# Performance work log

Hardware: AMD Instinct MI355X
Metric: run time of the kernel (lower is better)

## Reference

```python
import jax, jax.numpy as jnp
import numpy as np

# config (matches init_kwargs)
B, CIN, P, G = 8, 3, 16, 16          # batch, channels, patch, grid (img 256)
N = G * G                            # 256 tokens
D, NH, HD = 768, 12, 64              # hidden, heads, head_dim
L, E, K, HE = 4, 8, 2, 2048          # depth, experts, top_k, expert hidden
BN, FREQ = 128, 256                  # patch-embed bottleneck, timestep freq dim
EPS = 1e-6


def rms(x, w):
    return x * jax.lax.rsqrt(jnp.mean(x * x, axis=-1, keepdims=True) + EPS) * w


def rope_tables():
    # 2D RoPE: row/col grid coords, row-major token order
    half = HD // 2
    inv = 1.0 / (10000.0 ** (jnp.arange(0, half, 2, dtype=jnp.float32) / half))
    pos = jnp.arange(N)
    ph = (pos // G).astype(jnp.float32)
    pw = (pos % G).astype(jnp.float32)
    ah = jnp.repeat(ph[:, None] * inv, 2, axis=-1)   # (N, half)
    aw = jnp.repeat(pw[:, None] * inv, 2, axis=-1)
    ang = jnp.concatenate([ah, aw], axis=-1)          # (N, HD)
    return jnp.cos(ang)[None, None], jnp.sin(ang)[None, None]  # (1,1,N,HD)


def apply_rope(x, cos, sin):
    xp = x.reshape(*x.shape[:-1], HD // 2, 2)
    xr = jnp.stack([-xp[..., 1], xp[..., 0]], axis=-1).reshape(x.shape)
    return x * cos + xr * sin


def _forward(x, t, task_id, modality_id, pe1_w, pe1_b, pe2_w, pe2_b,
             t1_w, t1_b, t2_w, t2_b, task_tab, mod_tab,
             qkv_w, proj_w, qn_w, kn_w, norm1_w, norm2_w, adaln_w, adaln_b,
             router_w, moe_w1, moe_w2, moe_w3,
             fnorm_w, fada_w, fada_b, fproj_w, fproj_b):
    # PatchEmbed (bottleneck): conv(k=p,s=p) == linear over flattened (C,p,p) patches
    xp = x.reshape(B, CIN, G, P, G, P).transpose(0, 2, 4, 1, 3, 5).reshape(B, N, CIN * P * P)
    h = jax.nn.gelu(xp @ pe1_w + pe1_b, approximate=False) @ pe2_w + pe2_b  # (B,N,D)

    # TimestepEmbedder
    half = FREQ // 2
    freqs = jnp.exp(-jnp.log(10000.0) * jnp.arange(half, dtype=jnp.float32) / half)
    te = t[:, None] * freqs
    te = jnp.concatenate([jnp.cos(te), jnp.sin(te)], axis=-1)                # (B,FREQ)
    temb = jax.nn.silu(te @ t1_w + t1_b) @ t2_w + t2_b
    c = temb + task_tab[task_id] + mod_tab[modality_id]                      # (B,D)

    cos, sin = rope_tables()
    scale = 1.0 / np.sqrt(HD)

    def block(xb, p):
        qkvw, projw, qnw, knw, n1w, n2w, aw, ab, rw, w1, w2, w3 = p
        mod = (jax.nn.silu(c) @ aw + ab)[:, None, :]                         # (B,1,6D)
        sm, scm, gm, sp, scp, gp = jnp.split(mod, 6, axis=-1)
        # attention branch
        hh = rms(xb, n1w) * (1 + scm) + sm
        qkv = (hh @ qkvw).reshape(B, N, 3, NH, HD).transpose(2, 0, 3, 1, 4)
        q, k, v = qkv[0], qkv[1], qkv[2]                                     # (B,NH,N,HD)
        q = apply_rope(rms(q, qnw), cos, sin)
        k = apply_rope(rms(k, knw), cos, sin)
        att = jax.nn.softmax(jnp.einsum('bhnd,bhmd->bhnm', q, k) * scale, axis=-1)
        o = jnp.einsum('bhnm,bhmd->bhnd', att, v).transpose(0, 2, 1, 3).reshape(B, N, D)
        xb = xb + gm * (o @ projw)
        # MoE SwiGLU FFN branch: dense all-expert compute + gated combine
        hh = rms(xb, n2w) * (1 + scp) + sp
        hf = hh.reshape(B * N, D)
        logits = hf @ rw                                                     # (T,E)
        tv, ti = jax.lax.top_k(logits, K)
        gw = jax.nn.softmax(tv, axis=-1)                                     # (T,K)
        gates = jnp.sum(jax.nn.one_hot(ti, E, dtype=hf.dtype) * gw[..., None], axis=1)  # (T,E)
        h1 = jnp.einsum('td,edh->teh', hf, w1)
        h3 = jnp.einsum('td,edh->teh', hf, w3)
        y = jnp.einsum('teh,ehd->ted', jax.nn.silu(h1) * h3, w2)
        moe = jnp.einsum('ted,te->td', y, gates).reshape(B, N, D)
        xb = xb + gp * moe
        return xb, None

    params = (qkv_w, proj_w, qn_w, kn_w, norm1_w, norm2_w,
              adaln_w, adaln_b, router_w, moe_w1, moe_w2, moe_w3)
    h, _ = jax.lax.scan(block, h, params)

    fmod = (jax.nn.silu(c) @ fada_w + fada_b)[:, None, :]
    fs, fsc = jnp.split(fmod, 2, axis=-1)
    h = rms(h, fnorm_w) * (1 + fsc) + fs
    return h @ fproj_w + fproj_b                                             # (B,N,P*P*CIN)


def setup_inputs() -> dict:
    key = jax.random.key(0)
    ks = iter(jax.random.split(key, 40))
    r = lambda shape: jax.random.normal(next(ks), shape, jnp.float32) * 0.02
    return {
        'x': jax.random.normal(next(ks), (B, CIN, G * P, G * P), jnp.float32),
        't': jax.random.uniform(next(ks), (B,), jnp.float32) * 1000.0,
        'task_id': jax.random.randint(next(ks), (B,), 0, 2),
        'modality_id': jax.random.randint(next(ks), (B,), 0, 2),
        'pe1_w': r((CIN * P * P, BN)), 'pe1_b': jnp.zeros((BN,)),
        'pe2_w': r((BN, D)), 'pe2_b': jnp.zeros((D,)),
        't1_w': r((FREQ, D)), 't1_b': jnp.zeros((D,)),
        't2_w': r((D, D)), 't2_b': jnp.zeros((D,)),
        'task_tab': r((2, D)), 'mod_tab': r((2, D)),
        'qkv_w': r((L, D, 3 * D)), 'proj_w': r((L, D, D)),
        'qn_w': jnp.ones((L, HD)), 'kn_w': jnp.ones((L, HD)),
        'norm1_w': jnp.ones((L, D)), 'norm2_w': jnp.ones((L, D)),
        'adaln_w': r((L, D, 6 * D)), 'adaln_b': jnp.zeros((L, 6 * D)),
        'router_w': r((L, D, E)),
        'moe_w1': r((L, E, D, HE)), 'moe_w2': r((L, E, HE, D)), 'moe_w3': r((L, E, D, HE)),
        'fnorm_w': jnp.ones((D,)), 'fada_w': r((D, 2 * D)), 'fada_b': jnp.zeros((2 * D,)),
        'fproj_w': r((D, P * P * CIN)), 'fproj_b': jnp.zeros((P * P * CIN,)),
    }


def reference(x, t, task_id, modality_id, pe1_w, pe1_b, pe2_w, pe2_b,
              t1_w, t1_b, t2_w, t2_b, task_tab, mod_tab,
              qkv_w, proj_w, qn_w, kn_w, norm1_w, norm2_w, adaln_w, adaln_b,
              router_w, moe_w1, moe_w2, moe_w3,
              fnorm_w, fada_w, fada_b, fproj_w, fproj_b):
    return _forward(x, t, task_id, modality_id, pe1_w, pe1_b, pe2_w, pe2_b,
                    t1_w, t1_b, t2_w, t2_b, task_tab, mod_tab,
                    qkv_w, proj_w, qn_w, kn_w, norm1_w, norm2_w, adaln_w, adaln_b,
                    router_w, moe_w1, moe_w2, moe_w3,
                    fnorm_w, fada_w, fada_b, fproj_w, fproj_b)
```

## Files before the change

kernel.cpp:

```cpp
#include <hip/hip_runtime.h>
#include <hip/hip_bf16.h>
#include <math.h>

typedef __bf16 bf16x8 __attribute__((ext_vector_type(8)));
typedef float f32x4 __attribute__((ext_vector_type(4)));
typedef unsigned short ushort;

__device__ __forceinline__ float siluf(float x){ return x / (1.0f + expf(-x)); }
__device__ __forceinline__ float geluf(float x){ return 0.5f*x*(1.0f+erff(x*0.70710678118654752f)); }

__device__ __forceinline__ void split1(float f, ushort& hi, ushort& lo){
  union { float f; unsigned int u; } a; a.f = f;
  unsigned int h = a.u & 0xffff0000u;
  hi = (ushort)(h >> 16);
  union { unsigned int u; float f; } hf; hf.u = h;
  union { float f; unsigned int u; } l; l.f = f - hf.f;
  lo = (ushort)(l.u >> 16);
}
__device__ __forceinline__ void split2(float f0, float f1, unsigned int& hi, unsigned int& lo){
  union { float f; unsigned int u; } a, b; a.f = f0; b.f = f1;
  unsigned int h0 = a.u & 0xffff0000u, h1 = b.u & 0xffff0000u;
  hi = (h0 >> 16) | h1;
  union { unsigned int u; float f; } hf0, hf1; hf0.u = h0; hf1.u = h1;
  union { float f; unsigned int u; } l0, l1; l0.f = f0 - hf0.f; l1.f = f1 - hf1.f;
  lo = (l0.u >> 16) | (l1.u & 0xffff0000u);
}
__device__ __forceinline__ ushort f2bf(float f){
  union { float f; unsigned int u; } v; v.f = f;
  unsigned int r = v.u + 0x7fffu + ((v.u >> 16) & 1u);
  return (ushort)(r >> 16);
}

__global__ void k_patchify(const float* __restrict__ x,
                           ushort* __restrict__ xh, ushort* __restrict__ xl){
  int idx = blockIdx.x*256 + threadIdx.x;
  int t = idx / 768, f = idx % 768;
  int b = t >> 8, n = t & 255;
  int gh = n >> 4, gw = n & 15;
  int c = f >> 8, r = f & 255;
  int ph = r >> 4, pw = r & 15;
  float v = x[(((size_t)(b*3 + c)*256) + gh*16 + ph)*256 + gw*16 + pw];
  ushort h, l; split1(v, h, l);
  xh[idx] = h; xl[idx] = l;
}

__global__ __launch_bounds__(256) void k_cond(const float* __restrict__ t,
    const int* __restrict__ task_id, const int* __restrict__ mod_id,
    const float* __restrict__ t1w, const float* __restrict__ t1b,
    const float* __restrict__ t2w, const float* __restrict__ t2b,
    const float* __restrict__ task_tab, const float* __restrict__ mod_tab,
    float* __restrict__ c){
  __shared__ float te[256];
  __shared__ float tm[768];
  int b = blockIdx.x, tid = threadIdx.x;
  float tv = t[b];
  int i = tid & 127;
  float freq = expf(-9.210340371976184f * (float)i / 128.0f);
  float arg = tv * freq;
  te[tid] = (tid < 128) ? cosf(arg) : sinf(arg);
  __syncthreads();
  for (int d = tid; d < 768; d += 256){
    float acc = t1b[d];
    for (int k = 0; k < 256; k++) acc += te[k]*t1w[k*768+d];
    tm[d] = siluf(acc);
  }
  __syncthreads();
  for (int d = tid; d < 768; d += 256){
    float acc = t2b[d];
    for (int k = 0; k < 768; k++) acc += tm[k]*t2w[k*768+d];
    c[b*768+d] = acc + task_tab[task_id[b]*768+d] + mod_tab[mod_id[b]*768+d];
  }
}

__global__ __launch_bounds__(256) void k_mod(const float* __restrict__ c,
    const float* __restrict__ W, const float* __restrict__ bias,
    float* __restrict__ out, int N){
  __shared__ float sc[768];
  int b = blockIdx.y, tid = threadIdx.x;
  for (int k = tid; k < 768; k += 256) sc[k] = siluf(c[b*768+k]);
  __syncthreads();
  int n = blockIdx.x*256 + tid;
  float acc = bias[n];
  for (int k = 0; k < 768; k++) acc += sc[k]*W[(size_t)k*N + n];
  out[(size_t)b*N + n] = acc;
}

__global__ __launch_bounds__(256) void k_rms_mod(const float* __restrict__ x,
    float* __restrict__ out, ushort* __restrict__ oh, ushort* __restrict__ ol,
    const float* __restrict__ w,
    const float* __restrict__ shift, const float* __restrict__ scale, int mstride){
  __shared__ float red[256];
  int t = blockIdx.x, tid = threadIdx.x;
  float v0 = x[t*768 + tid], v1 = x[t*768 + 256 + tid], v2 = x[t*768 + 512 + tid];
  red[tid] = v0*v0 + v1*v1 + v2*v2;
  __syncthreads();
  for (int s2 = 128; s2 > 0; s2 >>= 1){ if (tid < s2) red[tid] += red[tid+s2]; __syncthreads(); }
  float r = rsqrtf(red[0]/768.0f + 1e-6f);
  int b = t >> 8;
  const float* sh = shift + (size_t)b*mstride;
  const float* scp = scale + (size_t)b*mstride;
  float o0 = v0*r*w[tid]    *(1.0f+scp[tid])     + sh[tid];
  float o1 = v1*r*w[tid+256]*(1.0f+scp[tid+256]) + sh[tid+256];
  float o2 = v2*r*w[tid+512]*(1.0f+scp[tid+512]) + sh[tid+512];
  out[t*768 + tid] = o0; out[t*768 + 256 + tid] = o1; out[t*768 + 512 + tid] = o2;
  ushort h, l;
  split1(o0, h, l); oh[t*768 + tid]       = h; ol[t*768 + tid]       = l;
  split1(o1, h, l); oh[t*768 + 256 + tid] = h; ol[t*768 + 256 + tid] = l;
  split1(o2, h, l); oh[t*768 + 512 + tid] = h; ol[t*768 + 512 + tid] = l;
}

__global__ __launch_bounds__(256) void k_qkv_prep(const float* __restrict__ qkv,
    ushort* __restrict__ qb, ushort* __restrict__ kb,
    const float* __restrict__ qnw, const float* __restrict__ knw){
  int t = blockIdx.x;
  int wid = threadIdx.x >> 6, lane = threadIdx.x & 63;
  int n = t & 255, b = t >> 8;
  float phc = (float)(n >> 4), pwc = (float)(n & 15);
  int j = (lane & 31) >> 1;
  float freq = expf(-9.210340371976184f * (float)j / 16.0f);
  float ang = ((lane < 32) ? phc : pwc) * freq;
  float ca = cosf(ang), sa = sinf(ang);
  for (int r = wid; r < 24; r += 4){
    int isK = (r >= 12);
    int h = isK ? r - 12 : r;
    const float* p = qkv + (size_t)t*2304 + (isK ? 768 : 0) + h*64 + lane;
    float v = *p;
    float ss = v*v;
    #pragma unroll
    for (int off = 32; off; off >>= 1) ss += __shfl_xor(ss, off);
    float rr = rsqrtf(ss/64.0f + 1e-6f);
    float w = isK ? knw[lane] : qnw[lane];
    float xn = v*rr*w;
    float partner = __shfl_xor(xn, 1);
    float xr = (lane & 1) ? partner : -partner;
    float res = xn*ca + xr*sa;
    if (!isK) res *= 0.125f;
    ushort* dst = (isK ? kb : qb) + ((size_t)(b*12 + h))*16384 + n*64 + lane;
    *dst = f2bf(res);
  }
}

__global__ __launch_bounds__(256) void k_vtrans(const float* __restrict__ qkv,
                                                ushort* __restrict__ vt){
  __shared__ float lds[64][65];
  int bh = blockIdx.x; int b = bh/12, h = bh%12;
  int tid = threadIdx.x;
  for (int p = 0; p < 4; p++){
    int n0 = p*64;
    __syncthreads();
    #pragma unroll
    for (int i = 0; i < 16; i++){
      int tt = i*4 + (tid>>6);
      int d = tid&63;
      lds[tt][d] = qkv[(size_t)(b*256 + n0 + tt)*2304 + 1536 + h*64 + d];
    }
    __syncthreads();
    #pragma unroll
    for (int i = 0; i < 16; i++){
      int d = i*4 + (tid>>6);
      int nn = tid&63;
      vt[(size_t)bh*16384 + d*256 + n0 + nn] = f2bf(lds[nn][d]);
    }
  }
}

#define KP 72
#define VP 264
__global__ __launch_bounds__(256) void k_fattn(
    const ushort* __restrict__ qb, const ushort* __restrict__ kb,
    const ushort* __restrict__ vt,
    ushort* __restrict__ oh, ushort* __restrict__ ol){
  __shared__ ushort ksh[256*KP];
  __shared__ ushort vsh[64*VP];
  __shared__ ushort psh[4][16*VP];
  int qt = blockIdx.x, bh = blockIdx.y;
  int b = bh/12, h = bh%12;
  int tid = threadIdx.x;
  #pragma unroll
  for (int it = 0; it < 8; it++){
    int idx = it*256 + tid;
    int row = idx >> 3, ch = idx & 7;
    *(uint4*)&ksh[row*KP + ch*8] = *(const uint4*)&kb[(size_t)bh*16384 + row*64 + ch*8];
  }
  #pragma unroll
  for (int it = 0; it < 8; it++){
    int idx = it*256 + tid;
    int row = idx >> 5, ch = idx & 31;
    *(uint4*)&vsh[row*VP + ch*8] = *(const uint4*)&vt[(size_t)bh*16384 + row*256 + ch*8];
  }
  __syncthreads();
  int lane = tid & 63, w = tid >> 6;
  int lr = lane & 15, lg = lane >> 4;
  int q0 = qt*64 + w*16;
  bf16x8 af0 = *(const bf16x8*)&qb[(size_t)bh*16384 + (q0 + lr)*64 + lg*8];
  bf16x8 af1 = *(const bf16x8*)&qb[(size_t)bh*16384 + (q0 + lr)*64 + lg*8 + 32];
  f32x4 s[16];
  #pragma unroll
  for (int nt = 0; nt < 16; nt++){
    f32x4 z = {};
    z = __builtin_amdgcn_mfma_f32_16x16x32_bf16(af0, *(const bf16x8*)&ksh[(nt*16 + lr)*KP + lg*8], z, 0, 0, 0);
    z = __builtin_amdgcn_mfma_f32_16x16x32_bf16(af1, *(const bf16x8*)&ksh[(nt*16 + lr)*KP + lg*8 + 32], z, 0, 0, 0);
    s[nt] = z;
  }
  float inv[4];
  #pragma unroll
  for (int r = 0; r < 4; r++){
    float m = -1e30f;
    #pragma unroll
    for (int nt = 0; nt < 16; nt++) m = fmaxf(m, s[nt][r]);
    #pragma unroll
    for (int off = 1; off < 16; off <<= 1) m = fmaxf(m, __shfl_xor(m, off));
    float sum = 0.f;
    #pragma unroll
    for (int nt = 0; nt < 16; nt++){ float p = expf(s[nt][r] - m); s[nt][r] = p; sum += p; }
    #pragma unroll
    for (int off = 1; off < 16; off <<= 1) sum += __shfl_xor(sum, off);
    inv[r] = 1.0f/sum;
  }
  #pragma unroll
  for (int nt = 0; nt < 16; nt++){
    #pragma unroll
    for (int r = 0; r < 4; r++)
      psh[w][(lg*4 + r)*VP + nt*16 + lr] = f2bf(s[nt][r]);
  }
  __syncthreads();
  f32x4 o[4] = {};
  #pragma unroll
  for (int dt = 0; dt < 4; dt++){
    #pragma unroll
    for (int k0 = 0; k0 < 8; k0++){
      bf16x8 pa = *(const bf16x8*)&psh[w][lr*VP + lg*8 + k0*32];
      bf16x8 bv = *(const bf16x8*)&vsh[(dt*16 + lr)*VP + lg*8 + k0*32];
      o[dt] = __builtin_amdgcn_mfma_f32_16x16x32_bf16(pa, bv, o[dt], 0, 0, 0);
    }
  }
  #pragma unroll
  for (int dt = 0; dt < 4; dt++){
    #pragma unroll
    for (int r = 0; r < 4; r++){
      int token = b*256 + q0 + lg*4 + r;
      int col = h*64 + dt*16 + lr;
      ushort hh, ll; split1(o[dt][r]*inv[lg*0 + r], hh, ll);
      oh[(size_t)token*768 + col] = hh;
      ol[(size_t)token*768 + col] = ll;
    }
  }
}

__global__ __launch_bounds__(256) void k_router(const float* __restrict__ hh,
    const float* __restrict__ rw, int* __restrict__ counts,
    int* __restrict__ list, float* __restrict__ gate_slot){
  int wid = threadIdx.x >> 6, lane = threadIdx.x & 63;
  int t = blockIdx.x*4 + wid;
  float acc[8] = {0,0,0,0,0,0,0,0};
  for (int k = lane; k < 768; k += 64){
    float a = hh[t*768 + k];
    #pragma unroll
    for (int e = 0; e < 8; e++) acc[e] += a * rw[k*8 + e];
  }
  #pragma unroll
  for (int e = 0; e < 8; e++){
    #pragma unroll
    for (int off = 32; off; off >>= 1) acc[e] += __shfl_xor(acc[e], off);
  }
  if (lane == 0){
    float v1 = -1e30f, v2 = -1e30f; int e1 = 0, e2 = 0;
    #pragma unroll
    for (int e = 0; e < 8; e++){
      float v = acc[e];
      if (v > v1){ v2 = v1; e2 = e1; v1 = v; e1 = e; }
      else if (v > v2){ v2 = v; e2 = e; }
    }
    float g1 = 1.0f/(1.0f+expf(v2-v1));
    float g2 = 1.0f - g1;
    int p1 = atomicAdd(&counts[e1], 1); list[e1*2048 + p1] = t*2;
    int p2 = atomicAdd(&counts[e2], 1); list[e2*2048 + p2] = t*2+1;
    gate_slot[t*2] = g1; gate_slot[t*2+1] = g2;
  }
}

#define LDK 40
template<int EPI>
__global__ __launch_bounds__(256) void gemm_split(
    const ushort* __restrict__ Ahi, const ushort* __restrict__ Alo,
    const float* __restrict__ B,
    float* __restrict__ C, ushort* __restrict__ Chi, ushort* __restrict__ Clo,
    int N, int K,
    const float* __restrict__ bias, const float* __restrict__ gate, int gstride){
  __shared__ ushort AsH[128*LDK], AsL[128*LDK];
  __shared__ ushort BsH[128*LDK], BsL[128*LDK];
  int tid = threadIdx.x;
  int m0 = blockIdx.y*128, n0 = blockIdx.x*128;
  int lane = tid & 63, wid = tid >> 6;
  int wr = wid >> 1, wc = wid & 1;
  int lr = lane & 15, lg = lane >> 4;
  int ar = tid & 127, ah = tid >> 7;
  int bn = tid & 127, bh = tid >> 7;
  size_t aoff = (size_t)(m0 + ar)*K + ah*16;
  f32x4 acc[4][4] = {};
  for (int k0 = 0; k0 < K; k0 += 32){
    { const uint4* ph = (const uint4*)(Ahi + aoff + k0);
      const uint4* pl = (const uint4*)(Alo + aoff + k0);
      uint4* qh = (uint4*)&AsH[ar*LDK + ah*16];
      uint4* ql = (uint4*)&AsL[ar*LDK + ah*16];
      qh[0] = ph[0]; qh[1] = ph[1]; ql[0] = pl[0]; ql[1] = pl[1]; }
    { const float* bp = B + (size_t)(k0 + bh*16)*N + n0 + bn;
      unsigned int* qh = (unsigned int*)&BsH[bn*LDK + bh*16];
      unsigned int* ql = (unsigned int*)&BsL[bn*LDK + bh*16];
      #pragma unroll
      for (int m2 = 0; m2 < 8; m2++){
        unsigned int h, l;
        split2(bp[(size_t)(2*m2)*N], bp[(size_t)(2*m2+1)*N], h, l);
        qh[m2] = h; ql[m2] = l;
      }
    }
    __syncthreads();
    bf16x8 aH[4], aL[4];
    #pragma unroll
    for (int mf = 0; mf < 4; mf++){
      aH[mf] = *(const bf16x8*)&AsH[(wr*64 + mf*16 + lr)*LDK + lg*8];
      aL[mf] = *(const bf16x8*)&AsL[(wr*64 + mf*16 + lr)*LDK + lg*8];
    }
    #pragma unroll
    for (int nf = 0; nf < 4; nf++){
      bf16x8 bH = *(const bf16x8*)&BsH[(wc*64 + nf*16 + lr)*LDK + lg*8];
      bf16x8 bL = *(const bf16x8*)&BsL[(wc*64 + nf*16 + lr)*LDK + lg*8];
      #pragma unroll
      for (int mf = 0; mf < 4; mf++){
        acc[mf][nf] = __builtin_amdgcn_mfma_f32_16x16x32_bf16(aH[mf], bH, acc[mf][nf], 0, 0, 0);
        acc[mf][nf] = __builtin_amdgcn_mfma_f32_16x16x32_bf16(aH[mf], bL, acc[mf][nf], 0, 0, 0);
        acc[mf][nf] = __builtin_amdgcn_mfma_f32_16x16x32_bf16(aL[mf], bH, acc[mf][nf], 0, 0, 0);
      }
    }
    __syncthreads();
  }
  #pragma unroll
  for (int mf = 0; mf < 4; mf++){
    #pragma unroll
    for (int nf = 0; nf < 4; nf++){
      #pragma unroll
      for (int r = 0; r < 4; r++){
        int m = m0 + wr*64 + mf*16 + lg*4 + r;
        int n = n0 + wc*64 + nf*16 + lr;
        float v = acc[mf][nf][r];
        if (EPI == 1){ C[(size_t)m*N + n] = v + bias[n]; }
        else if (EPI == 2){
          ushort h, l; split1(geluf(v + bias[n]), h, l);
          Chi[(size_t)m*N + n] = h; Clo[(size_t)m*N + n] = l;
        }
        else if (EPI == 3){ C[(size_t)m*N + n] += gate[(size_t)(m >> 8)*gstride + n]*v; }
        else { C[(size_t)m*N + n] = v; }
      }
    }
  }
}

__global__ __launch_bounds__(256) void moe_gemm1_split(
    const ushort* __restrict__ Ahi, const ushort* __restrict__ Alo,
    const float* __restrict__ w1, const float* __restrict__ w3,
    const int* __restrict__ counts, const int* __restrict__ list,
    ushort* __restrict__ mh, ushort* __restrict__ ml, int layer){
  int e = blockIdx.y >> 4, mt = blockIdx.y & 15;
  int count = counts[e];
  if (mt*128 >= count) return;
  __shared__ ushort AsH[128*LDK], AsL[128*LDK];
  __shared__ ushort B1H[128*LDK], B1L[128*LDK];
  __shared__ ushort B3H[128*LDK], B3L[128*LDK];
  __shared__ int slotArr[128];
  int tid = threadIdx.x;
  int n0 = blockIdx.x*128;
  const float* B1 = w1 + ((size_t)(layer*8 + e))*768*2048;
  const float* B3 = w3 + ((size_t)(layer*8 + e))*768*2048;
  if (tid < 128){
    int ml2 = mt*128 + tid;
    slotArr[tid] = (ml2 < count) ? list[e*2048 + ml2] : -1;
  }
  __syncthreads();
  int lane = tid & 63, wid = tid >> 6;
  int wr = wid >> 1, wc = wid & 1;
  int lr = lane & 15, lg = lane >> 4;
  int ar = tid & 127, ah = tid >> 7;
  int bn = tid & 127, bh = tid >> 7;
  int s0 = slotArr[ar]; int tok = (s0 < 0) ? 0 : (s0 >> 1);
  size_t aoff = (size_t)tok*768 + ah*16;
  f32x4 acc1[4][4] = {}, acc3[4][4] = {};
  for (int k0 = 0; k0 < 768; k0 += 32){
    { const uint4* ph = (const uint4*)(Ahi + aoff + k0);
      const uint4* pl = (const uint4*)(Alo + aoff + k0);
      uint4* qh = (uint4*)&AsH[ar*LDK + ah*16];
      uint4* ql = (uint4*)&AsL[ar*LDK + ah*16];
      qh[0] = ph[0]; qh[1] = ph[1]; ql[0] = pl[0]; ql[1] = pl[1]; }
    { const float* bp1 = B1 + (size_t)(k0 + bh*16)*2048 + n0 + bn;
      const float* bp3 = B3 + (size_t)(k0 + bh*16)*2048 + n0 + bn;
      unsigned int* q1h = (unsigned int*)&B1H[bn*LDK + bh*16];
      unsigned int* q1l = (unsigned int*)&B1L[bn*LDK + bh*16];
      unsigned int* q3h = (unsigned int*)&B3H[bn*LDK + bh*16];
      unsigned int* q3l = (unsigned int*)&B3L[bn*LDK + bh*16];
      #pragma unroll
      for (int m2 = 0; m2 < 8; m2++){
        unsigned int h, l;
        split2(bp1[(size_t)(2*m2)*2048], bp1[(size_t)(2*m2+1)*2048], h, l);
        q1h[m2] = h; q1l[m2] = l;
        split2(bp3[(size_t)(2*m2)*2048], bp3[(size_t)(2*m2+1)*2048], h, l);
        q3h[m2] = h; q3l[m2] = l;
      }
    }
    __syncthreads();
    bf16x8 aH[4], aL[4];
    #pragma unroll
    for (int mf = 0; mf < 4; mf++){
      aH[mf] = *(const bf16x8*)&AsH[(wr*64 + mf*16 + lr)*LDK + lg*8];
      aL[mf] = *(const bf16x8*)&AsL[(wr*64 + mf*16 + lr)*LDK + lg*8];
    }
    #pragma unroll
    for (int nf = 0; nf < 4; nf++){
      bf16x8 b1h = *(const bf16x8*)&B1H[(wc*64 + nf*16 + lr)*LDK + lg*8];
      bf16x8 b1l = *(const bf16x8*)&B1L[(wc*64 + nf*16 + lr)*LDK + lg*8];
      bf16x8 b3h = *(const bf16x8*)&B3H[(wc*64 + nf*16 + lr)*LDK + lg*8];
      bf16x8 b3l = *(const bf16x8*)&B3L[(wc*64 + nf*16 + lr)*LDK + lg*8];
      #pragma unroll
      for (int mf = 0; mf < 4; mf++){
        acc1[mf][nf] = __builtin_amdgcn_mfma_f32_16x16x32_bf16(aH[mf], b1h, acc1[mf][nf], 0, 0, 0);
        acc1[mf][nf] = __builtin_amdgcn_mfma_f32_16x16x32_bf16(aH[mf], b1l, acc1[mf][nf], 0, 0, 0);
        acc1[mf][nf] = __builtin_amdgcn_mfma_f32_16x16x32_bf16(aL[mf], b1h, acc1[mf][nf], 0, 0, 0);
        acc3[mf][nf] = __builtin_amdgcn_mfma_f32_16x16x32_bf16(aH[mf], b3h, acc3[mf][nf], 0, 0, 0);
        acc3[mf][nf] = __builtin_amdgcn_mfma_f32_16x16x32_bf16(aH[mf], b3l, acc3[mf][nf], 0, 0, 0);
        acc3[mf][nf] = __builtin_amdgcn_mfma_f32_16x16x32_bf16(aL[mf], b3h, acc3[mf][nf], 0, 0, 0);
      }
    }
    __syncthreads();
  }
  #pragma unroll
  for (int mf = 0; mf < 4; mf++){
    #pragma unroll
    for (int nf = 0; nf < 4; nf++){
      #pragma unroll
      for (int r = 0; r < 4; r++){
        int row = wr*64 + mf*16 + lg*4 + r;
        int sl = slotArr[row];
        if (sl < 0) continue;
        int n = n0 + wc*64 + nf*16 + lr;
        float v = siluf(acc1[mf][nf][r]) * acc3[mf][nf][r];
        ushort h, l; split1(v, h, l);
        mh[(size_t)sl*2048 + n] = h; ml[(size_t)sl*2048 + n] = l;
      }
    }
  }
}

__global__ __launch_bounds__(256) void moe_gemm2_split(
    const ushort* __restrict__ Ahi, const ushort* __restrict__ Alo,
    const float* __restrict__ w2,
    const int* __restrict__ counts, const int* __restrict__ list,
    float* __restrict__ y_slot, const float* __restrict__ gate_slot, int layer){
  int e = blockIdx.y >> 4, mt = blockIdx.y & 15;
  int count = counts[e];
  if (mt*128 >= count) return;
  __shared__ ushort AsH[128*LDK], AsL[128*LDK];
  __shared__ ushort BsH[128*LDK], BsL[128*LDK];
  __shared__ int slotArr[128];
  int tid = threadIdx.x;
  int n0 = blockIdx.x*128;
  const float* B = w2 + ((size_t)(layer*8 + e))*2048*768;
  if (tid < 128){
    int ml2 = mt*128 + tid;
    slotArr[tid] = (ml2 < count) ? list[e*2048 + ml2] : -1;
  }
  __syncthreads();
  int lane = tid & 63, wid = tid >> 6;
  int wr = wid >> 1, wc = wid & 1;
  int lr = lane & 15, lg = lane >> 4;
  int ar = tid & 127, ah = tid >> 7;
  int bn = tid & 127, bh = tid >> 7;
  int s0 = slotArr[ar]; int arow = (s0 < 0) ? 0 : s0;
  size_t aoff = (size_t)arow*2048 + ah*16;
  f32x4 acc[4][4] = {};
  for (int k0 = 0; k0 < 2048; k0 += 32){
    { const uint4* ph = (const uint4*)(Ahi + aoff + k0);
      const uint4* pl = (const uint4*)(Alo + aoff + k0);
      uint4* qh = (uint4*)&AsH[ar*LDK + ah*16];
      uint4* ql = (uint4*)&AsL[ar*LDK + ah*16];
      qh[0] = ph[0]; qh[1] = ph[1]; ql[0] = pl[0]; ql[1] = pl[1]; }
    { const float* bp = B + (size_t)(k0 + bh*16)*768 + n0 + bn;
      unsigned int* qh = (unsigned int*)&BsH[bn*LDK + bh*16];
      unsigned int* ql = (unsigned int*)&BsL[bn*LDK + bh*16];
      #pragma unroll
      for (int m2 = 0; m2 < 8; m2++){
        unsigned int h, l;
        split2(bp[(size_t)(2*m2)*768], bp[(size_t)(2*m2+1)*768], h, l);
        qh[m2] = h; ql[m2] = l;
      }
    }
    __syncthreads();
    bf16x8 aH[4], aL[4];
    #pragma unroll
    for (int mf = 0; mf < 4; mf++){
      aH[mf] = *(const bf16x8*)&AsH[(wr*64 + mf*16 + lr)*LDK + lg*8];
      aL[mf] = *(const bf16x8*)&AsL[(wr*64 + mf*16 + lr)*LDK + lg*8];
    }
    #pragma unroll
    for (int nf = 0; nf < 4; nf++){
      bf16x8 bH = *(const bf16x8*)&BsH[(wc*64 + nf*16 + lr)*LDK + lg*8];
      bf16x8 bL = *(const bf16x8*)&BsL[(wc*64 + nf*16 + lr)*LDK + lg*8];
      #pragma unroll
      for (int mf = 0; mf < 4; mf++){
        acc[mf][nf] = __builtin_amdgcn_mfma_f32_16x16x32_bf16(aH[mf], bH, acc[mf][nf], 0, 0, 0);
        acc[mf][nf] = __builtin_amdgcn_mfma_f32_16x16x32_bf16(aH[mf], bL, acc[mf][nf], 0, 0, 0);
        acc[mf][nf] = __builtin_amdgcn_mfma_f32_16x16x32_bf16(aL[mf], bH, acc[mf][nf], 0, 0, 0);
      }
    }
    __syncthreads();
  }
  #pragma unroll
  for (int mf = 0; mf < 4; mf++){
    #pragma unroll
    for (int nf = 0; nf < 4; nf++){
      #pragma unroll
      for (int r = 0; r < 4; r++){
        int row = wr*64 + mf*16 + lg*4 + r;
        int sl = slotArr[row];
        if (sl < 0) continue;
        int n = n0 + wc*64 + nf*16 + lr;
        y_slot[(size_t)sl*768 + n] = gate_slot[sl]*acc[mf][nf][r];
      }
    }
  }
}

__global__ void k_combine(float* __restrict__ x, const float* __restrict__ y_slot,
                          const float* __restrict__ gp){
  int idx = blockIdx.x*256 + threadIdx.x;
  int t = idx / 768, d = idx % 768;
  int b = t >> 8;
  x[idx] += gp[(size_t)b*4608 + d]*(y_slot[(size_t)(t*2)*768 + d] + y_slot[(size_t)(t*2+1)*768 + d]);
}

extern "C" void kernel_launch(void* const* d_in, const int* in_sizes, int n_in,
                              void* d_out, int out_size, void* d_ws, size_t ws_size,
                              hipStream_t stream){
  const float* x       = (const float*)d_in[0];
  const float* t       = (const float*)d_in[1];
  const int*   task_id = (const int*)d_in[2];
  const int*   mod_id  = (const int*)d_in[3];
  const float* pe1_w   = (const float*)d_in[4];
  const float* pe1_b   = (const float*)d_in[5];
  const float* pe2_w   = (const float*)d_in[6];
  const float* pe2_b   = (const float*)d_in[7];
  const float* t1_w    = (const float*)d_in[8];
  const float* t1_b    = (const float*)d_in[9];
  const float* t2_w    = (const float*)d_in[10];
  const float* t2_b    = (const float*)d_in[11];
  const float* task_tab= (const float*)d_in[12];
  const float* mod_tab = (const float*)d_in[13];
  const float* qkv_w   = (const float*)d_in[14];
  const float* proj_w  = (const float*)d_in[15];
  const float* qn_w    = (const float*)d_in[16];
  const float* kn_w    = (const float*)d_in[17];
  const float* n1_w    = (const float*)d_in[18];
  const float* n2_w    = (const float*)d_in[19];
  const float* ada_w   = (const float*)d_in[20];
  const float* ada_b   = (const float*)d_in[21];
  const float* rt_w    = (const float*)d_in[22];
  const float* w1      = (const float*)d_in[23];
  const float* w2      = (const float*)d_in[24];
  const float* w3      = (const float*)d_in[25];
  const float* fn_w    = (const float*)d_in[26];
  const float* fada_w  = (const float*)d_in[27];
  const float* fada_b  = (const float*)d_in[28];
  const float* fp_w    = (const float*)d_in[29];
  const float* fp_b    = (const float*)d_in[30];

  float* ws = (float*)d_ws;
  float* xbuf    = ws;  ws += (size_t)2048*768;
  float* hh      = ws;  ws += (size_t)2048*768;
  float* qkv     = ws;  ws += (size_t)2048*2304;
  float* y_slot  = ws;  ws += (size_t)4096*768;
  float* cbuf    = ws;  ws += 8*768;
  float* mod     = ws;  ws += 8*4608;
  float* fmod    = ws;  ws += 8*1536;
  float* gate_slot = ws; ws += 4096;
  int* counts = (int*)ws; ws += 8;
  int* list   = (int*)ws; ws += 8*2048;
  ws += 8;
  ushort* us = (ushort*)ws;
  ushort* hh_h   = us; us += (size_t)2048*768;
  ushort* hh_l   = us; us += (size_t)2048*768;
  ushort* hm_h   = us; us += (size_t)4096*2048;
  ushort* hm_l   = us; us += (size_t)4096*2048;
  ushort* attn_h = us; us += (size_t)2048*768;
  ushort* attn_l = us; us += (size_t)2048*768;
  ushort* qb     = us; us += (size_t)96*16384;
  ushort* kb     = us; us += (size_t)96*16384;
  ushort* vt     = us; us += (size_t)96*16384;
  ushort* xp_h  = hm_h;
  ushort* xp_l  = hm_h + (size_t)2048*768;
  ushort* pem_h = hm_l;
  ushort* pem_l = hm_l + (size_t)2048*128;

  k_patchify<<<6144, 256, 0, stream>>>(x, xp_h, xp_l);
  gemm_split<2><<<dim3(1, 16), 256, 0, stream>>>(xp_h, xp_l, pe1_w, nullptr, pem_h, pem_l, 128, 768, pe1_b, nullptr, 0);
  gemm_split<1><<<dim3(6, 16), 256, 0, stream>>>(pem_h, pem_l, pe2_w, xbuf, nullptr, nullptr, 768, 128, pe2_b, nullptr, 0);
  k_cond<<<8, 256, 0, stream>>>(t, task_id, mod_id, t1_w, t1_b, t2_w, t2_b, task_tab, mod_tab, cbuf);

  for (int l = 0; l < 4; l++){
    k_mod<<<dim3(18, 8), 256, 0, stream>>>(cbuf, ada_w + (size_t)l*768*4608, ada_b + (size_t)l*4608, mod, 4608);
    k_rms_mod<<<2048, 256, 0, stream>>>(xbuf, hh, hh_h, hh_l, n1_w + l*768, mod + 0, mod + 768, 4608);
    gemm_split<0><<<dim3(18, 16), 256, 0, stream>>>(hh_h, hh_l, qkv_w + (size_t)l*768*2304, qkv, nullptr, nullptr, 2304, 768, nullptr, nullptr, 0);
    k_qkv_prep<<<2048, 256, 0, stream>>>(qkv, qb, kb, qn_w + l*64, kn_w + l*64);
    k_vtrans<<<96, 256, 0, stream>>>(qkv, vt);
    k_fattn<<<dim3(4, 96), 256, 0, stream>>>(qb, kb, vt, attn_h, attn_l);
    gemm_split<3><<<dim3(6, 16), 256, 0, stream>>>(attn_h, attn_l, proj_w + (size_t)l*768*768, xbuf, nullptr, nullptr, 768, 768, nullptr, mod + 2*768, 4608);
    k_rms_mod<<<2048, 256, 0, stream>>>(xbuf, hh, hh_h, hh_l, n2_w + l*768, mod + 3*768, mod + 4*768, 4608);
    hipMemsetAsync(counts, 0, 8*sizeof(int), stream);
    k_router<<<512, 256, 0, stream>>>(hh, rt_w + (size_t)l*768*8, counts, list, gate_slot);
    moe_gemm1_split<<<dim3(16, 128), 256, 0, stream>>>(hh_h, hh_l, w1, w3, counts, list, hm_h, hm_l, l);
    moe_gemm2_split<<<dim3(6, 128), 256, 0, stream>>>(hm_h, hm_l, w2, counts, list, y_slot, gate_slot, l);
    k_combine<<<6144, 256, 0, stream>>>(xbuf, y_slot, mod + 5*768);
  }

  k_mod<<<dim3(6, 8), 256, 0, stream>>>(cbuf, fada_w, fada_b, fmod, 1536);
  k_rms_mod<<<2048, 256, 0, stream>>>(xbuf, hh, hh_h, hh_l, fn_w, fmod + 0, fmod + 768, 1536);
  gemm_split<1><<<dim3(6, 16), 256, 0, stream>>>(hh_h, hh_l, fp_w, (float*)d_out, nullptr, nullptr, 768, 768, fp_b, nullptr, 0);
}
```

Baseline: 2.844 ms.

## Pre-split weights into transposed bf16 hi/lo planes and restructure GEMMs

Adds a k_wsplit kernel that transposes each fp32 weight matrix and splits it into bf16 hi/lo planes in a workspace arena. The GEMMs then load pre-split, K-contiguous B tiles with vector loads instead of splitting strided fp32 columns inside every block. The GEMMs also drop the A tile in LDS, reading A fragments straight from global memory with 64-row M tiles. The QKV GEMM writes head-major hi/lo Q/K/V directly, removing the fp32 qkv and hh buffers. MoE weights are split two experts at a time, which adds more launches and an extra pass over weight memory on every call.

Result: slower. 6.811 ms (+139.5%).

```diff
diff --git a/kernel.cpp b/kernel.cpp
--- a/kernel.cpp
+++ b/kernel.cpp
@@ -6,9 +6,13 @@
 typedef float f32x4 __attribute__((ext_vector_type(4)));
 typedef unsigned short ushort;
 
+#define QOFF ((size_t)96*16384)
+
 __device__ __forceinline__ float siluf(float x){ return x / (1.0f + expf(-x)); }
 __device__ __forceinline__ float geluf(float x){ return 0.5f*x*(1.0f+erff(x*0.70710678118654752f)); }
-
+__device__ __forceinline__ float bf2f(ushort h){
+  union { unsigned int u; float f; } z; z.u = ((unsigned int)h) << 16; return z.f;
+}
 __device__ __forceinline__ void split1(float f, ushort& hi, ushort& lo){
   union { float f; unsigned int u; } a; a.f = f;
   unsigned int h = a.u & 0xffff0000u;
@@ -17,18 +21,33 @@
   union { float f; unsigned int u; } l; l.f = f - hf.f;
   lo = (ushort)(l.u >> 16);
 }
-__device__ __forceinline__ void split2(float f0, float f1, unsigned int& hi, unsigned int& lo){
-  union { float f; unsigned int u; } a, b; a.f = f0; b.f = f1;
-  unsigned int h0 = a.u & 0xffff0000u, h1 = b.u & 0xffff0000u;
-  hi = (h0 >> 16) | h1;
-  union { unsigned int u; float f; } hf0, hf1; hf0.u = h0; hf1.u = h1;
-  union { float f; unsigned int u; } l0, l1; l0.f = f0 - hf0.f; l1.f = f1 - hf1.f;
-  lo = (l0.u >> 16) | (l1.u & 0xffff0000u);
-}
 __device__ __forceinline__ ushort f2bf(float f){
   union { float f; unsigned int u; } v; v.f = f;
   unsigned int r = v.u + 0x7fffu + ((v.u >> 16) & 1u);
   return (ushort)(r >> 16);
+}
+
+__global__ __launch_bounds__(256) void k_wsplit(const float* __restrict__ src,
+    ushort* __restrict__ dstH, ushort* __restrict__ dstL, int K, int N){
+  __shared__ float lds[64][65];
+  int n0 = blockIdx.x*64, k0 = blockIdx.y*64;
+  size_t zb = (size_t)blockIdx.z*K*N;
+  int tid = threadIdx.x;
+  int c = tid & 63, rq = tid >> 6;
+  #pragma unroll
+  for (int i = 0; i < 16; i++){
+    int kk = i*4 + rq;
+    lds[kk][c] = src[zb + (size_t)(k0+kk)*N + n0 + c];
+  }
+  __syncthreads();
+  #pragma unroll
+  for (int i = 0; i < 16; i++){
+    int nn = i*4 + rq;
+    float v = lds[c][nn];
+    ushort h, l; split1(v, h, l);
+    dstH[zb + (size_t)(n0+nn)*K + k0 + c] = h;
+    dstL[zb + (size_t)(n0+nn)*K + k0 + c] = l;
+  }
 }
 
 __global__ void k_patchify(const float* __restrict__ x,
@@ -86,7 +105,7 @@
 }
 
 __global__ __launch_bounds__(256) void k_rms_mod(const float* __restrict__ x,
-    float* __restrict__ out, ushort* __restrict__ oh, ushort* __restrict__ ol,
+    ushort* __restrict__ oh, ushort* __restrict__ ol,
     const float* __restrict__ w,
     const float* __restrict__ shift, const float* __restrict__ scale, int mstride){
   __shared__ float red[256];
@@ -102,15 +121,13 @@
   float o0 = v0*r*w[tid]    *(1.0f+scp[tid])     + sh[tid];
   float o1 = v1*r*w[tid+256]*(1.0f+scp[tid+256]) + sh[tid+256];
   float o2 = v2*r*w[tid+512]*(1.0f+scp[tid+512]) + sh[tid+512];
-  out[t*768 + tid] = o0; out[t*768 + 256 + tid] = o1; out[t*768 + 512 + tid] = o2;
   ushort h, l;
   split1(o0, h, l); oh[t*768 + tid]       = h; ol[t*768 + tid]       = l;
   split1(o1, h, l); oh[t*768 + 256 + tid] = h; ol[t*768 + 256 + tid] = l;
   split1(o2, h, l); oh[t*768 + 512 + tid] = h; ol[t*768 + 512 + tid] = l;
 }
 
-__global__ __launch_bounds__(256) void k_qkv_prep(const float* __restrict__ qkv,
-    ushort* __restrict__ qb, ushort* __restrict__ kb,
+__global__ __launch_bounds__(256) void k_qkv_prep(ushort* __restrict__ qp, ushort* __restrict__ kp,
     const float* __restrict__ qnw, const float* __restrict__ knw){
   int t = blockIdx.x;
   int wid = threadIdx.x >> 6, lane = threadIdx.x & 63;
@@ -123,8 +140,8 @@
   for (int r = wid; r < 24; r += 4){
     int isK = (r >= 12);
     int h = isK ? r - 12 : r;
-    const float* p = qkv + (size_t)t*2304 + (isK ? 768 : 0) + h*64 + lane;
-    float v = *p;
+    ushort* p = (isK ? kp : qp) + ((size_t)(b*12 + h))*16384 + n*64 + lane;
+    float v = bf2f(p[0]) + bf2f(p[QOFF]);
     float ss = v*v;
     #pragma unroll
     for (int off = 32; off; off >>= 1) ss += __shfl_xor(ss, off);
@@ -135,15 +152,14 @@
     float xr = (lane & 1) ? partner : -partner;
     float res = xn*ca + xr*sa;
     if (!isK) res *= 0.125f;
-    ushort* dst = (isK ? kb : qb) + ((size_t)(b*12 + h))*16384 + n*64 + lane;
-    *dst = f2bf(res);
-  }
-}
-
-__global__ __launch_bounds__(256) void k_vtrans(const float* __restrict__ qkv,
+    *p = f2bf(res);
+  }
+}
+
+__global__ __launch_bounds__(256) void k_vtrans(const ushort* __restrict__ vp,
                                                 ushort* __restrict__ vt){
   __shared__ float lds[64][65];
-  int bh = blockIdx.x; int b = bh/12, h = bh%12;
+  int bh = blockIdx.x;
   int tid = threadIdx.x;
   for (int p = 0; p < 4; p++){
     int n0 = p*64;
@@ -152,7 +168,8 @@
     for (int i = 0; i < 16; i++){
       int tt = i*4 + (tid>>6);
       int d = tid&63;
-      lds[tt][d] = qkv[(size_t)(b*256 + n0 + tt)*2304 + 1536 + h*64 + d];
+      size_t idx = (size_t)bh*16384 + (n0 + tt)*64 + d;
+      lds[tt][d] = bf2f(vp[idx]) + bf2f(vp[idx + QOFF]);
     }
     __syncthreads();
     #pragma unroll
@@ -240,21 +257,22 @@
     for (int r = 0; r < 4; r++){
       int token = b*256 + q0 + lg*4 + r;
       int col = h*64 + dt*16 + lr;
-      ushort hh, ll; split1(o[dt][r]*inv[lg*0 + r], hh, ll);
+      ushort hh, ll; split1(o[dt][r]*inv[r], hh, ll);
       oh[(size_t)token*768 + col] = hh;
       ol[(size_t)token*768 + col] = ll;
     }
   }
 }
 
-__global__ __launch_bounds__(256) void k_router(const float* __restrict__ hh,
+__global__ __launch_bounds__(256) void k_router(const ushort* __restrict__ hh_h,
+    const ushort* __restrict__ hh_l,
     const float* __restrict__ rw, int* __restrict__ counts,
     int* __restrict__ list, float* __restrict__ gate_slot){
   int wid = threadIdx.x >> 6, lane = threadIdx.x & 63;
   int t = blockIdx.x*4 + wid;
   float acc[8] = {0,0,0,0,0,0,0,0};
   for (int k = lane; k < 768; k += 64){
-    float a = hh[t*768 + k];
+    float a = bf2f(hh_h[(size_t)t*768 + k]) + bf2f(hh_l[(size_t)t*768 + k]);
     #pragma unroll
     for (int e = 0; e < 8; e++) acc[e] += a * rw[k*8 + e];
   }
@@ -279,164 +297,158 @@
   }
 }
 
-#define LDK 40
+#define LDKB 40
 template<int EPI>
-__global__ __launch_bounds__(256) void gemm_split(
-    const ushort* __restrict__ Ahi, const ushort* __restrict__ Alo,
-    const float* __restrict__ B,
-    float* __restrict__ C, ushort* __restrict__ Chi, ushort* __restrict__ Clo,
+__global__ __launch_bounds__(256) void gemm_ps(
+    const ushort* __restrict__ Ah, const ushort* __restrict__ Al,
+    const ushort* __restrict__ Bth, const ushort* __restrict__ Btl,
+    float* __restrict__ C, ushort* __restrict__ Ch, ushort* __restrict__ Cl,
+    ushort* __restrict__ Cv,
     int N, int K,
     const float* __restrict__ bias, const float* __restrict__ gate, int gstride){
-  __shared__ ushort AsH[128*LDK], AsL[128*LDK];
-  __shared__ ushort BsH[128*LDK], BsL[128*LDK];
+  __shared__ ushort BsH[128*LDKB], BsL[128*LDKB];
   int tid = threadIdx.x;
-  int m0 = blockIdx.y*128, n0 = blockIdx.x*128;
+  int m0 = blockIdx.y*64, n0 = blockIdx.x*128;
   int lane = tid & 63, wid = tid >> 6;
   int wr = wid >> 1, wc = wid & 1;
   int lr = lane & 15, lg = lane >> 4;
-  int ar = tid & 127, ah = tid >> 7;
-  int bn = tid & 127, bh = tid >> 7;
-  size_t aoff = (size_t)(m0 + ar)*K + ah*16;
-  f32x4 acc[4][4] = {};
+  int brow = tid & 127, bh2 = tid >> 7;
+  const ushort* bth = Bth + (size_t)(n0 + brow)*K + bh2*16;
+  const ushort* btl = Btl + (size_t)(n0 + brow)*K + bh2*16;
+  size_t ar0 = (size_t)(m0 + wr*32 + lr)*K + lg*8;
+  size_t ar1 = (size_t)(m0 + wr*32 + 16 + lr)*K + lg*8;
+  f32x4 acc[2][4] = {};
   for (int k0 = 0; k0 < K; k0 += 32){
-    { const uint4* ph = (const uint4*)(Ahi + aoff + k0);
-      const uint4* pl = (const uint4*)(Alo + aoff + k0);
-      uint4* qh = (uint4*)&AsH[ar*LDK + ah*16];
-      uint4* ql = (uint4*)&AsL[ar*LDK + ah*16];
-      qh[0] = ph[0]; qh[1] = ph[1]; ql[0] = pl[0]; ql[1] = pl[1]; }
-    { const float* bp = B + (size_t)(k0 + bh*16)*N + n0 + bn;
-      unsigned int* qh = (unsigned int*)&BsH[bn*LDK + bh*16];
-      unsigned int* ql = (unsigned int*)&BsL[bn*LDK + bh*16];
-      #pragma unroll
-      for (int m2 = 0; m2 < 8; m2++){
-        unsigned int h, l;
-        split2(bp[(size_t)(2*m2)*N], bp[(size_t)(2*m2+1)*N], h, l);
-        qh[m2] = h; ql[m2] = l;
-      }
-    }
-    __syncthreads();
-    bf16x8 aH[4], aL[4];
-    #pragma unroll
-    for (int mf = 0; mf < 4; mf++){
-      aH[mf] = *(const bf16x8*)&AsH[(wr*64 + mf*16 + lr)*LDK + lg*8];
-      aL[mf] = *(const bf16x8*)&AsL[(wr*64 + mf*16 + lr)*LDK + lg*8];
-    }
+    bf16x8 a0h = *(const bf16x8*)(Ah + ar0 + k0);
+    bf16x8 a0l = *(const bf16x8*)(Al + ar0 + k0);
+    bf16x8 a1h = *(const bf16x8*)(Ah + ar1 + k0);
+    bf16x8 a1l = *(const bf16x8*)(Al + ar1 + k0);
+    *(uint4*)&BsH[brow*LDKB + bh2*16]     = *(const uint4*)(bth + k0);
+    *(uint4*)&BsH[brow*LDKB + bh2*16 + 8] = *(const uint4*)(bth + k0 + 8);
+    *(uint4*)&BsL[brow*LDKB + bh2*16]     = *(const uint4*)(btl + k0);
+    *(uint4*)&BsL[brow*LDKB + bh2*16 + 8] = *(const uint4*)(btl + k0 + 8);
+    __syncthreads();
     #pragma unroll
     for (int nf = 0; nf < 4; nf++){
-      bf16x8 bH = *(const bf16x8*)&BsH[(wc*64 + nf*16 + lr)*LDK + lg*8];
-      bf16x8 bL = *(const bf16x8*)&BsL[(wc*64 + nf*16 + lr)*LDK + lg*8];
-      #pragma unroll
-      for (int mf = 0; mf < 4; mf++){
-        acc[mf][nf] = __builtin_amdgcn_mfma_f32_16x16x32_bf16(aH[mf], bH, acc[mf][nf], 0, 0, 0);
-        acc[mf][nf] = __builtin_amdgcn_mfma_f32_16x16x32_bf16(aH[mf], bL, acc[mf][nf], 0, 0, 0);
-        acc[mf][nf] = __builtin_amdgcn_mfma_f32_16x16x32_bf16(aL[mf], bH, acc[mf][nf], 0, 0, 0);
-      }
-    }
-    __syncthreads();
-  }
-  #pragma unroll
-  for (int mf = 0; mf < 4; mf++){
+      bf16x8 bH = *(const bf16x8*)&BsH[(wc*64 + nf*16 + lr)*LDKB + lg*8];
+      bf16x8 bL = *(const bf16x8*)&BsL[(wc*64 + nf*16 + lr)*LDKB + lg*8];
+      acc[0][nf] = __builtin_amdgcn_mfma_f32_16x16x32_bf16(a0h, bH, acc[0][nf], 0, 0, 0);
+      acc[0][nf] = __builtin_amdgcn_mfma_f32_16x16x32_bf16(a0h, bL, acc[0][nf], 0, 0, 0);
+      acc[0][nf] = __builtin_amdgcn_mfma_f32_16x16x32_bf16(a0l, bH, acc[0][nf], 0, 0, 0);
+      acc[1][nf] = __builtin_amdgcn_mfma_f32_16x16x32_bf16(a1h, bH, acc[1][nf], 0, 0, 0);
+      acc[1][nf] = __builtin_amdgcn_mfma_f32_16x16x32_bf16(a1h, bL, acc[1][nf], 0, 0, 0);
+      acc[1][nf] = __builtin_amdgcn_mfma_f32_16x16x32_bf16(a1l, bH, acc[1][nf], 0, 0, 0);
+    }
+    __syncthreads();
+  }
+  #pragma unroll
+  for (int mf = 0; mf < 2; mf++){
     #pragma unroll
     for (int nf = 0; nf < 4; nf++){
       #pragma unroll
       for (int r = 0; r < 4; r++){
-        int m = m0 + wr*64 + mf*16 + lg*4 + r;
+        int m = m0 + wr*32 + mf*16 + lg*4 + r;
         int n = n0 + wc*64 + nf*16 + lr;
         float v = acc[mf][nf][r];
         if (EPI == 1){ C[(size_t)m*N + n] = v + bias[n]; }
         else if (EPI == 2){
           ushort h, l; split1(geluf(v + bias[n]), h, l);
-          Chi[(size_t)m*N + n] = h; Clo[(size_t)m*N + n] = l;
+          Ch[(size_t)m*N + n] = h; Cl[(size_t)m*N + n] = l;
         }
         else if (EPI == 3){ C[(size_t)m*N + n] += gate[(size_t)(m >> 8)*gstride + n]*v; }
+        else if (EPI == 4){
+          int sec = n / 768;
+          int hn = n - sec*768;
+          int hd = hn >> 6, d = hn & 63;
+          int bb = m >> 8, nn = m & 255;
+          ushort* base = (sec == 0) ? Ch : (sec == 1) ? Cl : Cv;
+          size_t idx = ((size_t)(bb*12 + hd))*16384 + nn*64 + d;
+          ushort h, l; split1(v, h, l);
+          base[idx] = h; base[idx + QOFF] = l;
+        }
         else { C[(size_t)m*N + n] = v; }
       }
     }
   }
 }
 
-__global__ __launch_bounds__(256) void moe_gemm1_split(
-    const ushort* __restrict__ Ahi, const ushort* __restrict__ Alo,
-    const float* __restrict__ w1, const float* __restrict__ w3,
+__global__ __launch_bounds__(256) void moe_gemm1_ps(
+    const ushort* __restrict__ Ah, const ushort* __restrict__ Al,
+    const ushort* __restrict__ w1Th, const ushort* __restrict__ w1Tl,
+    const ushort* __restrict__ w3Th, const ushort* __restrict__ w3Tl,
     const int* __restrict__ counts, const int* __restrict__ list,
-    ushort* __restrict__ mh, ushort* __restrict__ ml, int layer){
-  int e = blockIdx.y >> 4, mt = blockIdx.y & 15;
+    ushort* __restrict__ mh, ushort* __restrict__ ml, int ebase){
+  int le = blockIdx.x >> 5, mt = blockIdx.x & 31;
+  int e = ebase + le;
   int count = counts[e];
-  if (mt*128 >= count) return;
-  __shared__ ushort AsH[128*LDK], AsL[128*LDK];
-  __shared__ ushort B1H[128*LDK], B1L[128*LDK];
-  __shared__ ushort B3H[128*LDK], B3L[128*LDK];
-  __shared__ int slotArr[128];
+  if (mt*64 >= count) return;
+  __shared__ ushort B1H[128*LDKB], B1L[128*LDKB];
+  __shared__ ushort B3H[128*LDKB], B3L[128*LDKB];
+  __shared__ int slotArr[64];
   int tid = threadIdx.x;
-  int n0 = blockIdx.x*128;
-  const float* B1 = w1 + ((size_t)(layer*8 + e))*768*2048;
-  const float* B3 = w3 + ((size_t)(layer*8 + e))*768*2048;
-  if (tid < 128){
-    int ml2 = mt*128 + tid;
+  int n0 = blockIdx.y*128;
+  if (tid < 64){
+    int ml2 = mt*64 + tid;
     slotArr[tid] = (ml2 < count) ? list[e*2048 + ml2] : -1;
   }
   __syncthreads();
   int lane = tid & 63, wid = tid >> 6;
   int wr = wid >> 1, wc = wid & 1;
   int lr = lane & 15, lg = lane >> 4;
-  int ar = tid & 127, ah = tid >> 7;
-  int bn = tid & 127, bh = tid >> 7;
-  int s0 = slotArr[ar]; int tok = (s0 < 0) ? 0 : (s0 >> 1);
-  size_t aoff = (size_t)tok*768 + ah*16;
-  f32x4 acc1[4][4] = {}, acc3[4][4] = {};
+  int brow = tid & 127, bh2 = tid >> 7;
+  size_t eoff = (size_t)le*2048*768;
+  const ushort* b1h = w1Th + eoff + (size_t)(n0 + brow)*768 + bh2*16;
+  const ushort* b1l = w1Tl + eoff + (size_t)(n0 + brow)*768 + bh2*16;
+  const ushort* b3h = w3Th + eoff + (size_t)(n0 + brow)*768 + bh2*16;
+  const ushort* b3l = w3Tl + eoff + (size_t)(n0 + brow)*768 + bh2*16;
+  int s0a = slotArr[wr*32 + lr];      int tok0 = (s0a < 0) ? 0 : (s0a >> 1);
+  int s1a = slotArr[wr*32 + 16 + lr]; int tok1 = (s1a < 0) ? 0 : (s1a >> 1);
+  size_t ar0 = (size_t)tok0*768 + lg*8;
+  size_t ar1 = (size_t)tok1*768 + lg*8;
+  f32x4 acc1[2][4] = {}, acc3[2][4] = {};
   for (int k0 = 0; k0 < 768; k0 += 32){
-    { const uint4* ph = (const uint4*)(Ahi + aoff + k0);
-      const uint4* pl = (const uint4*)(Alo + aoff + k0);
-      uint4* qh = (uint4*)&AsH[ar*LDK + ah*16];
-      uint4* ql = (uint4*)&AsL[ar*LDK + ah*16];
-      qh[0] = ph[0]; qh[1] = ph[1]; ql[0] = pl[0]; ql[1] = pl[1]; }
-    { const float* bp1 = B1 + (size_t)(k0 + bh*16)*2048 + n0 + bn;
-      const float* bp3 = B3 + (size_t)(k0 + bh*16)*2048 + n0 + bn;
-      unsigned int* q1h = (unsigned int*)&B1H[bn*LDK + bh*16];
-      unsigned int* q1l = (unsigned int*)&B1L[bn*LDK + bh*16];
-      unsigned int* q3h = (unsigned int*)&B3H[bn*LDK + bh*16];
-      unsigned int* q3l = (unsigned int*)&B3L[bn*LDK + bh*16];
-      #pragma unroll
-      for (int m2 = 0; m2 < 8; m2++){
-        unsigned int h, l;
-        split2(bp1[(size_t)(2*m2)*2048], bp1[(size_t)(2*m2+1)*2048], h, l);
-        q1h[m2] = h; q1l[m2] = l;
-        split2(bp3[(size_t)(2*m2)*2048], bp3[(size_t)(2*m2+1)*2048], h, l);
-        q3h[m2] = h; q3l[m2] = l;
-      }
-    }
-    __syncthreads();
-    bf16x8 aH[4], aL[4];
-    #pragma unroll
-    for (int mf = 0; mf < 4; mf++){
-      aH[mf] = *(const bf16x8*)&AsH[(wr*64 + mf*16 + lr)*LDK + lg*8];
-      aL[mf] = *(const bf16x8*)&AsL[(wr*64 + mf*16 + lr)*LDK + lg*8];
-    }
+    bf16x8 a0h = *(const bf16x8*)(Ah + ar0 + k0);
+    bf16x8 a0l = *(const bf16x8*)(Al + ar0 + k0);
+    bf16x8 a1h = *(const bf16x8*)(Ah + ar1 + k0);
+    bf16x8 a1l = *(const bf16x8*)(Al + ar1 + k0);
+    *(uint4*)&B1H[brow*LDKB + bh2*16]     = *(const uint4*)(b1h + k0);
+    *(uint4*)&B1H[brow*LDKB + bh2*16 + 8] = *(const uint4*)(b1h + k0 + 8);
+    *(uint4*)&B1L[brow*LDKB + bh2*16]     = *(const uint4*)(b1l + k0);
+    *(uint4*)&B1L[brow*LDKB + bh2*16 + 8] = *(const uint4*)(b1l + k0 + 8);
+    *(uint4*)&B3H[brow*LDKB + bh2*16]     = *(const uint4*)(b3h + k0);
+    *(uint4*)&B3H[brow*LDKB + bh2*16 + 8] = *(const uint4*)(b3h + k0 + 8);
+    *(uint4*)&B3L[brow*LDKB + bh2*16]     = *(const uint4*)(b3l + k0);
+    *(uint4*)&B3L[brow*LDKB + bh2*16 + 8] = *(const uint4*)(b3l + k0 + 8);
+    __syncthreads();
     #pragma unroll
     for (int nf = 0; nf < 4; nf++){
-      bf16x8 b1h = *(const bf16x8*)&B1H[(wc*64 + nf*16 + lr)*LDK + lg*8];
-      bf16x8 b1l = *(const bf16x8*)&B1L[(wc*64 + nf*16 + lr)*LDK + lg*8];
-      bf16x8 b3h = *(const bf16x8*)&B3H[(wc*64 + nf*16 + lr)*LDK + lg*8];
-      bf16x8 b3l = *(const bf16x8*)&B3L[(wc*64 + nf*16 + lr)*LDK + lg*8];
-      #pragma unroll
-      for (int mf = 0; mf < 4; mf++){
-        acc1[mf][nf] = __builtin_amdgcn_mfma_f32_16x16x32_bf16(aH[mf], b1h, acc1[mf][nf], 0, 0, 0);
-        acc1[mf][nf] = __builtin_amdgcn_mfma_f32_16x16x32_bf16(aH[mf], b1l, acc1[mf][nf], 0, 0, 0);
-        acc1[mf][nf] = __builtin_amdgcn_mfma_f32_16x16x32_bf16(aL[mf], b1h, acc1[mf][nf], 0, 0, 0);
-        acc3[mf][nf] = __builtin_amdgcn_mfma_f32_16x16x32_bf16(aH[mf], b3h, acc3[mf][nf], 0, 0, 0);
-        acc3[mf][nf] = __builtin_amdgcn_mfma_f32_16x16x32_bf16(aH[mf], b3l, acc3[mf][nf], 0, 0, 0);
-        acc3[mf][nf] = __builtin_amdgcn_mfma_f32_16x16x32_bf16(aL[mf], b3h, acc3[mf][nf], 0, 0, 0);
-      }
-    }
-    __syncthreads();
-  }
-  #pragma unroll
-  for (int mf = 0; mf < 4; mf++){
+      int boff = (wc*64 + nf*16 + lr)*LDKB + lg*8;
+      bf16x8 c1h = *(const bf16x8*)&B1H[boff];
+      bf16x8 c1l = *(const bf16x8*)&B1L[boff];
+      bf16x8 c3h = *(const bf16x8*)&B3H[boff];
+      bf16x8 c3l = *(const bf16x8*)&B3L[boff];
+      acc1[0][nf] = __builtin_amdgcn_mfma_f32_16x16x32_bf16(a0h, c1h, acc1[0][nf], 0, 0, 0);
+      acc1[0][nf] = __builtin_amdgcn_mfma_f32_16x16x32_bf16(a0h, c1l, acc1[0][nf], 0, 0, 0);
+      acc1[0][nf] = __builtin_amdgcn_mfma_f32_16x16x32_bf16(a0l, c1h, acc1[0][nf], 0, 0, 0);
+      acc1[1][nf] = __builtin_amdgcn_mfma_f32_16x16x32_bf16(a1h, c1h, acc1[1][nf], 0, 0, 0);
+      acc1[1][nf] = __builtin_amdgcn_mfma_f32_16x16x32_bf16(a1h, c1l, acc1[1][nf], 0, 0, 0);
+      acc1[1][nf] = __builtin_amdgcn_mfma_f32_16x16x32_bf16(a1l, c1h, acc1[1][nf], 0, 0, 0);
+      acc3[0][nf] = __builtin_amdgcn_mfma_f32_16x16x32_bf16(a0h, c3h, acc3[0][nf], 0, 0, 0);
+      acc3[0][nf] = __builtin_amdgcn_mfma_f32_16x16x32_bf16(a0h, c3l, acc3[0][nf], 0, 0, 0);
+      acc3[0][nf] = __builtin_amdgcn_mfma_f32_16x16x32_bf16(a0l, c3h, acc3[0][nf], 0, 0, 0);
+      acc3[1][nf] = __builtin_amdgcn_mfma_f32_16x16x32_bf16(a1h, c3h, acc3[1][nf], 0, 0, 0);
+      acc3[1][nf] = __builtin_amdgcn_mfma_f32_16x16x32_bf16(a1h, c3l, acc3[1][nf], 0, 0, 0);
+      acc3[1][nf] = __builtin_amdgcn_mfma_f32_16x16x32_bf16(a1l, c3h, acc3[1][nf], 0, 0, 0);
+    }
+    __syncthreads();
+  }
+  #pragma unroll
+  for (int mf = 0; mf < 2; mf++){
     #pragma unroll
     for (int nf = 0; nf < 4; nf++){
       #pragma unroll
       for (int r = 0; r < 4; r++){
-        int row = wr*64 + mf*16 + lg*4 + r;
+        int row = wr*32 + mf*16 + lg*4 + r;
         int sl = slotArr[row];
         if (sl < 0) continue;
         int n = n0 + wc*64 + nf*16 + lr;
@@ -448,76 +460,66 @@
   }
 }
 
-__global__ __launch_bounds__(256) void moe_gemm2_split(
-    const ushort* __restrict__ Ahi, const ushort* __restrict__ Alo,
-    const float* __restrict__ w2,
+__global__ __launch_bounds__(256) void moe_gemm2_ps(
+    const ushort* __restrict__ Ah, const ushort* __restrict__ Al,
+    const ushort* __restrict__ w2Th, const ushort* __restrict__ w2Tl,
     const int* __restrict__ counts, const int* __restrict__ list,
-    float* __restrict__ y_slot, const float* __restrict__ gate_slot, int layer){
-  int e = blockIdx.y >> 4, mt = blockIdx.y & 15;
+    float* __restrict__ y_slot, const float* __restrict__ gate_slot, int ebase){
+  int le = blockIdx.x >> 5, mt = blockIdx.x & 31;
+  int e = ebase + le;
   int count = counts[e];
-  if (mt*128 >= count) return;
-  __shared__ ushort AsH[128*LDK], AsL[128*LDK];
-  __shared__ ushort BsH[128*LDK], BsL[128*LDK];
-  __shared__ int slotArr[128];
+  if (mt*64 >= count) return;
+  __shared__ ushort BsH[128*LDKB], BsL[128*LDKB];
+  __shared__ int slotArr[64];
   int tid = threadIdx.x;
-  int n0 = blockIdx.x*128;
-  const float* B = w2 + ((size_t)(layer*8 + e))*2048*768;
-  if (tid < 128){
-    int ml2 = mt*128 + tid;
+  int n0 = blockIdx.y*128;
+  if (tid < 64){
+    int ml2 = mt*64 + tid;
     slotArr[tid] = (ml2 < count) ? list[e*2048 + ml2] : -1;
   }
   __syncthreads();
   int lane = tid & 63, wid = tid >> 6;
   int wr = wid >> 1, wc = wid & 1;
   int lr = lane & 15, lg = lane >> 4;
-  int ar = tid & 127, ah = tid >> 7;
-  int bn = tid & 127, bh = tid >> 7;
-  int s0 = slotArr[ar]; int arow = (s0 < 0) ? 0 : s0;
-  size_t aoff = (size_t)arow*2048 + ah*16;
-  f32x4 acc[4][4] = {};
+  int brow = tid & 127, bh2 = tid >> 7;
+  size_t eoff = (size_t)le*768*2048;
+  const ushort* bth = w2Th + eoff + (size_t)(n0 + brow)*2048 + bh2*16;
+  const ushort* btl = w2Tl + eoff + (size_t)(n0 + brow)*2048 + bh2*16;
+  int s0a = slotArr[wr*32 + lr];      int sa0 = (s0a < 0) ? 0 : s0a;
+  int s1a = slotArr[wr*32 + 16 + lr]; int sa1 = (s1a < 0) ? 0 : s1a;
+  size_t ar0 = (size_t)sa0*2048 + lg*8;
+  size_t ar1 = (size_t)sa1*2048 + lg*8;
+  f32x4 acc[2][4] = {};
   for (int k0 = 0; k0 < 2048; k0 += 32){
-    { const uint4* ph = (const uint4*)(Ahi + aoff + k0);
-      const uint4* pl = (const uint4*)(Alo + aoff + k0);
-      uint4* qh = (uint4*)&AsH[ar*LDK + ah*16];
-      uint4* ql = (uint4*)&AsL[ar*LDK + ah*16];
-      qh[0] = ph[0]; qh[1] = ph[1]; ql[0] = pl[0]; ql[1] = pl[1]; }
-    { const float* bp = B + (size_t)(k0 + bh*16)*768 + n0 + bn;
-      unsigned int* qh = (unsigned int*)&BsH[bn*LDK + bh*16];
-      unsigned int* ql = (unsigned int*)&BsL[bn*LDK + bh*16];
-      #pragma unroll
-      for (int m2 = 0; m2 < 8; m2++){
-        unsigned int h, l;
-        split2(bp[(size_t)(2*m2)*768], bp[(size_t)(2*m2+1)*768], h, l);
-        qh[m2] = h; ql[m2] = l;
-      }
-    }
-    __syncthreads();
-    bf16x8 aH[4], aL[4];
-    #pragma unroll
-    for (int mf = 0; mf < 4; mf++){
-      aH[mf] = *(const bf16x8*)&AsH[(wr*64 + mf*16 + lr)*LDK + lg*8];
-      aL[mf] = *(const bf16x8*)&AsL[(wr*64 + mf*16 + lr)*LDK + lg*8];
-    }
+    bf16x8 a0h = *(const bf16x8*)(Ah + ar0 + k0);
+    bf16x8 a0l = *(const bf16x8*)(Al + ar0 + k0);
+    bf16x8 a1h = *(const bf16x8*)(Ah + ar1 + k0);
+    bf16x8 a1l = *(const bf16x8*)(Al + ar1 + k0);
+    *(uint4*)&BsH[brow*LDKB + bh2*16]     = *(const uint4*)(bth + k0);
+    *(uint4*)&BsH[brow*LDKB + bh2*16 + 8] = *(const uint4*)(bth + k0 + 8);
+    *(uint4*)&BsL[brow*LDKB + bh2*16]     = *(const uint4*)(btl + k0);
+    *(uint4*)&BsL[brow*LDKB + bh2*16 + 8] = *(const uint4*)(btl + k0 + 8);
+    __syncthreads();
     #pragma unroll
     for (int nf = 0; nf < 4; nf++){
-      bf16x8 bH = *(const bf16x8*)&BsH[(wc*64 + nf*16 + lr)*LDK + lg*8];
-      bf16x8 bL = *(const bf16x8*)&BsL[(wc*64 + nf*16 + lr)*LDK + lg*8];
-      #pragma unroll
-      for (int mf = 0; mf < 4; mf++){
-        acc[mf][nf] = __builtin_amdgcn_mfma_f32_16x16x32_bf16(aH[mf], bH, acc[mf][nf], 0, 0, 0);
-        acc[mf][nf] = __builtin_amdgcn_mfma_f32_16x16x32_bf16(aH[mf], bL, acc[mf][nf], 0, 0, 0);
-        acc[mf][nf] = __builtin_amdgcn_mfma_f32_16x16x32_bf16(aL[mf], bH, acc[mf][nf], 0, 0, 0);
-      }
-    }
-    __syncthreads();
-  }
-  #pragma unroll
-  for (int mf = 0; mf < 4; mf++){
+      bf16x8 bH = *(const bf16x8*)&BsH[(wc*64 + nf*16 + lr)*LDKB + lg*8];
+      bf16x8 bL = *(const bf16x8*)&BsL[(wc*64 + nf*16 + lr)*LDKB + lg*8];
+      acc[0][nf] = __builtin_amdgcn_mfma_f32_16x16x32_bf16(a0h, bH, acc[0][nf], 0, 0, 0);
+      acc[0][nf] = __builtin_amdgcn_mfma_f32_16x16x32_bf16(a0h, bL, acc[0][nf], 0, 0, 0);
+      acc[0][nf] = __builtin_amdgcn_mfma_f32_16x16x32_bf16(a0l, bH, acc[0][nf], 0, 0, 0);
+      acc[1][nf] = __builtin_amdgcn_mfma_f32_16x16x32_bf16(a1h, bH, acc[1][nf], 0, 0, 0);
+      acc[1][nf] = __builtin_amdgcn_mfma_f32_16x16x32_bf16(a1h, bL, acc[1][nf], 0, 0, 0);
+      acc[1][nf] = __builtin_amdgcn_mfma_f32_16x16x32_bf16(a1l, bH, acc[1][nf], 0, 0, 0);
+    }
+    __syncthreads();
+  }
+  #pragma unroll
+  for (int mf = 0; mf < 2; mf++){
     #pragma unroll
     for (int nf = 0; nf < 4; nf++){
       #pragma unroll
       for (int r = 0; r < 4; r++){
-        int row = wr*64 + mf*16 + lg*4 + r;
+        int row = wr*32 + mf*16 + lg*4 + r;
         int sl = slotArr[row];
         if (sl < 0) continue;
         int n = n0 + wc*64 + nf*16 + lr;
@@ -572,9 +574,6 @@
 
   float* ws = (float*)d_ws;
   float* xbuf    = ws;  ws += (size_t)2048*768;
-  float* hh      = ws;  ws += (size_t)2048*768;
-  float* qkv     = ws;  ws += (size_t)2048*2304;
-  float* y_slot  = ws;  ws += (size_t)4096*768;
   float* cbuf    = ws;  ws += 8*768;
   float* mod     = ws;  ws += 8*4608;
   float* fmod    = ws;  ws += 8*1536;
@@ -589,36 +588,65 @@
   ushort* hm_l   = us; us += (size_t)4096*2048;
   ushort* attn_h = us; us += (size_t)2048*768;
   ushort* attn_l = us; us += (size_t)2048*768;
-  ushort* qb     = us; us += (size_t)96*16384;
-  ushort* kb     = us; us += (size_t)96*16384;
   ushort* vt     = us; us += (size_t)96*16384;
+  ushort* arena  = us; us += (size_t)8*2048*768;
+
+  const size_t PLANE = (size_t)2048*768;
+  ushort* aw1h = arena;
+  ushort* aw1l = arena + 2*PLANE;
+  ushort* aw3h = arena + 4*PLANE;
+  ushort* aw3l = arena + 6*PLANE;
+  ushort* aw2h = arena;
+  ushort* aw2l = arena + 2*PLANE;
+  ushort* aqh  = arena;
+  ushort* aql  = arena + (size_t)2304*768;
+  ushort* aph  = arena;
+  ushort* apl  = arena + (size_t)768*768;
+  float*  y_slot = (float*)(arena + 4*PLANE);
+  ushort* q_pair = hm_h;
+  ushort* k_pair = hm_h + 2*QOFF;
+  ushort* v_pair = hm_l;
   ushort* xp_h  = hm_h;
   ushort* xp_l  = hm_h + (size_t)2048*768;
   ushort* pem_h = hm_l;
   ushort* pem_l = hm_l + (size_t)2048*128;
 
   k_patchify<<<6144, 256, 0, stream>>>(x, xp_h, xp_l);
-  gemm_split<2><<<dim3(1, 16), 256, 0, stream>>>(xp_h, xp_l, pe1_w, nullptr, pem_h, pem_l, 128, 768, pe1_b, nullptr, 0);
-  gemm_split<1><<<dim3(6, 16), 256, 0, stream>>>(pem_h, pem_l, pe2_w, xbuf, nullptr, nullptr, 768, 128, pe2_b, nullptr, 0);
+  k_wsplit<<<dim3(2, 12, 1), 256, 0, stream>>>(pe1_w, aqh, aql, 768, 128);
+  gemm_ps<2><<<dim3(1, 32), 256, 0, stream>>>(xp_h, xp_l, aqh, aql, nullptr, pem_h, pem_l, nullptr, 128, 768, pe1_b, nullptr, 0);
+  k_wsplit<<<dim3(12, 2, 1), 256, 0, stream>>>(pe2_w, aqh, aql, 128, 768);
+  gemm_ps<1><<<dim3(6, 32), 256, 0, stream>>>(pem_h, pem_l, aqh, aql, xbuf, nullptr, nullptr, nullptr, 768, 128, pe2_b, nullptr, 0);
   k_cond<<<8, 256, 0, stream>>>(t, task_id, mod_id, t1_w, t1_b, t2_w, t2_b, task_tab, mod_tab, cbuf);
 
   for (int l = 0; l < 4; l++){
     k_mod<<<dim3(18, 8), 256, 0, stream>>>(cbuf, ada_w + (size_t)l*768*4608, ada_b + (size_t)l*4608, mod, 4608);
-    k_rms_mod<<<2048, 256, 0, stream>>>(xbuf, hh, hh_h, hh_l, n1_w + l*768, mod + 0, mod + 768, 4608);
-    gemm_split<0><<<dim3(18, 16), 256, 0, stream>>>(hh_h, hh_l, qkv_w + (size_t)l*768*2304, qkv, nullptr, nullptr, 2304, 768, nullptr, nullptr, 0);
-    k_qkv_prep<<<2048, 256, 0, stream>>>(qkv, qb, kb, qn_w + l*64, kn_w + l*64);
-    k_vtrans<<<96, 256, 0, stream>>>(qkv, vt);
-    k_fattn<<<dim3(4, 96), 256, 0, stream>>>(qb, kb, vt, attn_h, attn_l);
-    gemm_split<3><<<dim3(6, 16), 256, 0, stream>>>(attn_h, attn_l, proj_w + (size_t)l*768*768, xbuf, nullptr, nullptr, 768, 768, nullptr, mod + 2*768, 4608);
-    k_rms_mod<<<2048, 256, 0, stream>>>(xbuf, hh, hh_h, hh_l, n2_w + l*768, mod + 3*768, mod + 4*768, 4608);
+    k_rms_mod<<<2048, 256, 0, stream>>>(xbuf, hh_h, hh_l, n1_w + l*768, mod + 0, mod + 768, 4608);
+    k_wsplit<<<dim3(36, 12, 1), 256, 0, stream>>>(qkv_w + (size_t)l*768*2304, aqh, aql, 768, 2304);
+    gemm_ps<4><<<dim3(18, 32), 256, 0, stream>>>(hh_h, hh_l, aqh, aql, nullptr, q_pair, k_pair, v_pair, 2304, 768, nullptr, nullptr, 0);
+    k_qkv_prep<<<2048, 256, 0, stream>>>(q_pair, k_pair, qn_w + l*64, kn_w + l*64);
+    k_vtrans<<<96, 256, 0, stream>>>(v_pair, vt);
+    k_fattn<<<dim3(4, 96), 256, 0, stream>>>(q_pair, k_pair, vt, attn_h, attn_l);
+    k_wsplit<<<dim3(12, 12, 1), 256, 0, stream>>>(proj_w + (size_t)l*768*768, aph, apl, 768, 768);
+    gemm_ps<3><<<dim3(6, 32), 256, 0, stream>>>(attn_h, attn_l, aph, apl, xbuf, nullptr, nullptr, nullptr, 768, 768, nullptr, mod + 2*768, 4608);
+    k_rms_mod<<<2048, 256, 0, stream>>>(xbuf, hh_h, hh_l, n2_w + l*768, mod + 3*768, mod + 4*768, 4608);
     hipMemsetAsync(counts, 0, 8*sizeof(int), stream);
-    k_router<<<512, 256, 0, stream>>>(hh, rt_w + (size_t)l*768*8, counts, list, gate_slot);
-    moe_gemm1_split<<<dim3(16, 128), 256, 0, stream>>>(hh_h, hh_l, w1, w3, counts, list, hm_h, hm_l, l);
-    moe_gemm2_split<<<dim3(6, 128), 256, 0, stream>>>(hm_h, hm_l, w2, counts, list, y_slot, gate_slot, l);
+    k_router<<<512, 256, 0, stream>>>(hh_h, hh_l, rt_w + (size_t)l*768*8, counts, list, gate_slot);
+    for (int g = 0; g < 4; g++){
+      int ebase = g*2;
+      k_wsplit<<<dim3(32, 12, 2), 256, 0, stream>>>(w1 + ((size_t)(l*8 + ebase))*768*2048, aw1h, aw1l, 768, 2048);
+      k_wsplit<<<dim3(32, 12, 2), 256, 0, stream>>>(w3 + ((size_t)(l*8 + ebase))*768*2048, aw3h, aw3l, 768, 2048);
+      moe_gemm1_ps<<<dim3(64, 16), 256, 0, stream>>>(hh_h, hh_l, aw1h, aw1l, aw3h, aw3l, counts, list, hm_h, hm_l, ebase);
+    }
+    for (int g = 0; g < 4; g++){
+      int ebase = g*2;
+      k_wsplit<<<dim3(12, 32, 2), 256, 0, stream>>>(w2 + ((size_t)(l*8 + ebase))*2048*768, aw2h, aw2l, 2048, 768);
+      moe_gemm2_ps<<<dim3(64, 6), 256, 0, stream>>>(hm_h, hm_l, aw2h, aw2l, counts, list, y_slot, gate_slot, ebase);
+    }
     k_combine<<<6144, 256, 0, stream>>>(xbuf, y_slot, mod + 5*768);
   }
 
   k_mod<<<dim3(6, 8), 256, 0, stream>>>(cbuf, fada_w, fada_b, fmod, 1536);
-  k_rms_mod<<<2048, 256, 0, stream>>>(xbuf, hh, hh_h, hh_l, fn_w, fmod + 0, fmod + 768, 1536);
-  gemm_split<1><<<dim3(6, 16), 256, 0, stream>>>(hh_h, hh_l, fp_w, (float*)d_out, nullptr, nullptr, 768, 768, fp_b, nullptr, 0);
-}
+  k_rms_mod<<<2048, 256, 0, stream>>>(xbuf, hh_h, hh_l, fn_w, fmod + 0, fmod + 768, 1536);
+  k_wsplit<<<dim3(12, 12, 1), 256, 0, stream>>>(fp_w, aph, apl, 768, 768);
+  gemm_ps<1><<<dim3(6, 32), 256, 0, stream>>>(hh_h, hh_l, aph, apl, (float*)d_out, nullptr, nullptr, nullptr, 768, 768, fp_b, nullptr, 0);
+}
```
